# Performance work log

Measured on AMD Instinct MI355X. Metric: run time of the kernel, lower is better.

## Reference

```python
import jax, jax.numpy as jnp
import numpy as np

EMBED_DIM = 256
NUM_CODES = 8192
COMMIT_COST = 0.25


def setup_inputs() -> dict:
    key = jax.random.key(0)
    k1, k2 = jax.random.split(key)
    x = jax.random.normal(k1, (16, 1024, EMBED_DIM), dtype=jnp.float32)
    # torch init is uniform(-1/K, 1/K); use small-scale normal-like init via uniform
    codebook = jax.random.uniform(k2, (NUM_CODES, EMBED_DIM), dtype=jnp.float32,
                                  minval=-1.0 / NUM_CODES, maxval=1.0 / NUM_CODES)
    return {"x": x, "codebook": codebook}


def reference(x, codebook):
    # x: [B, S, D], codebook: [K, D]
    input_shape = x.shape
    flat = x.reshape(-1, EMBED_DIM)  # [N, D]
    distances = (jnp.sum(flat * flat, axis=1, keepdims=True)
                 + jnp.sum(codebook * codebook, axis=1)
                 - 2.0 * jnp.matmul(flat, codebook.T))
    encoding_indices = jnp.argmin(distances, axis=1)  # [N]
    # one-hot @ codebook is just a gather
    quantized = jnp.take(codebook, encoding_indices, axis=0).reshape(input_shape)
    # training w/ EMA: commitment loss only (codebook updated via EMA buffers, not grad)
    commitment_loss = COMMIT_COST * jnp.mean(
        (jax.lax.stop_gradient(quantized) - x) ** 2)
    # straight-through estimator
    quantized_st = x + jax.lax.stop_gradient(quantized - x)
    indices = encoding_indices.reshape(input_shape[:-1])
    return quantized_st, indices, commitment_loss
```

## Files before the change

### kernel.cpp

```cpp
#include <hip/hip_runtime.h>

#define D 256
#define KCODES 8192
#define NTOK 16384
#define QSIZE (NTOK * D)
#define NBLK 128
#define CBS 64
#define TH 2e-4f
#define CBSCALE 4096.0f
#define UNSCALE2 4.8828125e-4f
#define CCAP 4096

typedef _Float16 f16x8 __attribute__((ext_vector_type(8)));
typedef float f32x4 __attribute__((ext_vector_type(4)));
typedef __attribute__((address_space(3))) void* lds_vp;
typedef __attribute__((address_space(1))) const void* gbl_vp;

#define P1_LDS (128 * 256 * 2 + 2 * 128 * 32 * 2)
#define P2_LDS (256 * 65 * 4)

__device__ __forceinline__ ushort f32_to_bf16(float f) {
    unsigned u = __float_as_uint(f);
    return (ushort)((u + 0x7FFFu + ((u >> 16) & 1)) >> 16);
}
__device__ __forceinline__ float bf16_to_f32(ushort h) {
    return __uint_as_float((unsigned)h << 16);
}
__device__ __forceinline__ ushort f32_to_f16(float f) {
    _Float16 h = (_Float16)f;
    ushort u; __builtin_memcpy(&u, &h, 2);
    return u;
}
__device__ __forceinline__ float rdlane(float v, int lane) {
    return __uint_as_float(__builtin_amdgcn_readlane(__float_as_uint(v), lane));
}

__global__ __launch_bounds__(256) void prep_kernel(
    const float* __restrict__ x, ushort* __restrict__ xb,
    float* __restrict__ xsq, const float* __restrict__ cb,
    float* __restrict__ e2, unsigned* __restrict__ counts) {
    const int bid = blockIdx.x;
    const int tid = threadIdx.x;
    if (bid == 0 && tid < NBLK) counts[tid] = 0;
    if (bid < 4096) {
        int i = bid * 256 + tid;
        float4 v = reinterpret_cast<const float4*>(x)[i];
        ushort4 o;
        o.x = f32_to_f16(v.x); o.y = f32_to_f16(v.y);
        o.z = f32_to_f16(v.z); o.w = f32_to_f16(v.w);
        reinterpret_cast<ushort4*>(xb)[i] = o;
        float s = v.x * v.x + v.y * v.y + v.z * v.z + v.w * v.w;
#pragma unroll
        for (int off = 32; off > 0; off >>= 1) s += __shfl_down(s, off);
        if ((tid & 63) == 0) xsq[i >> 6] = s;
    } else {
        int c = (bid - 4096) * 4 + (tid >> 6);
        int lane = tid & 63;
        float4 v = reinterpret_cast<const float4*>(cb + (size_t)c * D)[lane];
        float s = v.x * v.x + v.y * v.y + v.z * v.z + v.w * v.w;
#pragma unroll
        for (int off = 32; off > 0; off >>= 1) s += __shfl_down(s, off);
        if (lane == 0) e2[c] = s;
    }
}

__global__ __launch_bounds__(256, 2) void pass1_kernel(
    const ushort* __restrict__ xb, const float* __restrict__ cb,
    const float* __restrict__ e2, unsigned* __restrict__ screen) {
    extern __shared__ ushort sm[];
    ushort* Bsh = sm;
    ushort* Ash = sm + 128 * 256;
    const int tid = threadIdx.x;
    const int w = tid >> 6, l = tid & 63;
    const int wr = w >> 1, wc = w & 1;
    const int n0 = blockIdx.y * 128;
    const int tc0 = blockIdx.x * (NTOK / 8);

#pragma unroll
    for (int j = 0; j < 16; ++j) {
        int c = tid + j * 256;
        int row = c >> 5, slot = c & 31;
        const float4* grow = reinterpret_cast<const float4*>(cb + (size_t)(n0 + row) * D);
        float4 f0 = grow[slot * 2];
        float4 f1 = grow[slot * 2 + 1];
        uint4 q;
        q.x = (unsigned)f32_to_f16(f0.x * CBSCALE) |
              ((unsigned)f32_to_f16(f0.y * CBSCALE) << 16);
        q.y = (unsigned)f32_to_f16(f0.z * CBSCALE) |
              ((unsigned)f32_to_f16(f0.w * CBSCALE) << 16);
        q.z = (unsigned)f32_to_f16(f1.x * CBSCALE) |
              ((unsigned)f32_to_f16(f1.y * CBSCALE) << 16);
        q.w = (unsigned)f32_to_f16(f1.z * CBSCALE) |
              ((unsigned)f32_to_f16(f1.w * CBSCALE) << 16);
        int sw = slot ^ (row & 7);
        *reinterpret_cast<uint4*>(Bsh + row * 256 + sw * 8) = q;
    }

    const int arow0 = w * 32 + (l >> 2);
    const int arow1 = arow0 + 16;
    const int asg8 = (((l & 3) ^ ((l >> 3) & 3)) << 3);

#define STAGE_A(TB, KT, BUF)                                                               \
    do {                                                                                   \
        __builtin_amdgcn_global_load_lds(                                                  \
            (gbl_vp)(xb + (size_t)((TB) + arow0) * D + (KT) * 32 + asg8),                  \
            (lds_vp)(Ash + (BUF) * 4096 + w * 1024), 16, 0, 0);                            \
        __builtin_amdgcn_global_load_lds(                                                  \
            (gbl_vp)(xb + (size_t)((TB) + arow1) * D + (KT) * 32 + asg8),                  \
            (lds_vp)(Ash + (BUF) * 4096 + w * 1024 + 512), 16, 0, 0);                      \
    } while (0)

    const int qh = l >> 4, l7 = l & 7, lm = l & 15;
    const int aslot = qh ^ ((lm >> 1) & 3);
    const int arow_rd = (wr * 64 + lm) * 32 + aslot * 8;
    const int brow_rd = (wc * 64 + lm) * 256;

    float e2v[16];
#pragma unroll
    for (int cm = 0; cm < 4; ++cm)
#pragma unroll
        for (int r = 0; r < 4; ++r)
            e2v[cm * 4 + r] = e2[n0 + wc * 64 + cm * 16 + qh * 4 + r];
    const int nb64 = blockIdx.y * 2 + wc;

    STAGE_A(tc0, 0, 0);
    __syncthreads();

    for (int tt = 0; tt < 16; ++tt) {
        const int tbase = tc0 + tt * 128;
        f32x4 acc[4][4];
#pragma unroll
        for (int cm = 0; cm < 4; ++cm)
#pragma unroll
            for (int tn = 0; tn < 4; ++tn) acc[cm][tn] = (f32x4)0.f;
#pragma unroll
        for (int kt = 0; kt < 8; ++kt) {
            const int cur = kt & 1;
            if (kt < 7) STAGE_A(tbase, kt + 1, cur ^ 1);
            else if (tt < 15) STAGE_A(tbase + 128, 0, cur ^ 1);
            const ushort* abase = Ash + cur * 4096 + arow_rd;
            f16x8 a[4], b[4];
#pragma unroll
            for (int tn = 0; tn < 4; ++tn)
                a[tn] = *reinterpret_cast<const f16x8*>(abase + tn * 512);
#pragma unroll
            for (int cm = 0; cm < 4; ++cm)
                b[cm] = *reinterpret_cast<const f16x8*>(
                    Bsh + brow_rd + cm * 4096 + (((kt * 4 + qh) ^ l7) << 3));
#pragma unroll
            for (int cm = 0; cm < 4; ++cm)
#pragma unroll
                for (int tn = 0; tn < 4; ++tn)
                    acc[cm][tn] = __builtin_amdgcn_mfma_f32_16x16x32_f16(
                        b[cm], a[tn], acc[cm][tn], 0, 0, 0);
            if (kt == 7) {
#pragma unroll
                for (int tn = 0; tn < 4; ++tn) {
                    float v1 = fmaf(-UNSCALE2, acc[0][tn][0], e2v[0]);
                    float v2 = 3.4e38f;
                    int a1 = qh * 4;
#pragma unroll
                    for (int q = 1; q < 16; ++q) {
                        const int cm = q >> 2, r = q & 3;
                        float f = fmaf(-UNSCALE2, acc[cm][tn][r], e2v[q]);
                        int idx = cm * 16 + qh * 4 + r;
                        bool lt = f < v1;
                        v2 = lt ? v1 : fminf(v2, f);
                        a1 = lt ? idx : a1;
                        v1 = lt ? f : v1;
                    }
#pragma unroll
                    for (int off = 16; off < 64; off <<= 1) {
                        float ov1 = __shfl_xor(v1, off);
                        float ov2 = __shfl_xor(v2, off);
                        int oa1 = __shfl_xor(a1, off);
                        float nv2 = fminf(fminf(v2, ov2), fmaxf(v1, ov1));
                        bool take = ov1 < v1;
                        v1 = take ? ov1 : v1;
                        a1 = take ? oa1 : a1;
                        v2 = nv2;
                    }
                    if (qh == 0) {
                        int token = tbase + wr * 64 + tn * 16 + lm;
                        ushort m1b = f32_to_bf16(v1);
                        unsigned big = (v2 - bf16_to_f32(m1b) > TH) ? 1u : 0u;
                        screen[(size_t)token * NBLK + nb64] =
                            ((unsigned)m1b << 16) | ((unsigned)a1 << 1) | big;
                    }
                }
            }
            __syncthreads();
        }
    }
#undef STAGE_A
}

__global__ __launch_bounds__(256) void pass2a_kernel(
    const unsigned* __restrict__ screen, unsigned long long* __restrict__ bestKey,
    unsigned* __restrict__ cand, unsigned* __restrict__ counts,
    float* __restrict__ out) {
    const int tid = threadIdx.x;
    const int w = tid >> 6, l = tid & 63;
    const int token = blockIdx.x * 4 + w;
    if (blockIdx.x == 0 && tid == 0) out[(size_t)QSIZE + NTOK] = 0.f;

    uint2 u2 = reinterpret_cast<const uint2*>(screen + (size_t)token * NBLK)[l];
    float ma = bf16_to_f32((ushort)(u2.x >> 16));
    float mb = bf16_to_f32((ushort)(u2.y >> 16));
    float v1, v2; unsigned pk; int blk;
    if (mb < ma) { v1 = mb; v2 = ma; pk = u2.y; blk = 2 * l + 1; }
    else         { v1 = ma; v2 = mb; pk = u2.x; blk = 2 * l; }
#pragma unroll
    for (int off = 1; off < 64; off <<= 1) {
        float ov1 = __shfl_xor(v1, off);
        float ov2 = __shfl_xor(v2, off);
        unsigned opk = __shfl_xor(pk, off);
        int oblk = __shfl_xor(blk, off);
        float nv2 = fminf(fminf(v2, ov2), fmaxf(v1, ov1));
        bool take = ov1 < v1;
        v1 = take ? ov1 : v1;
        pk = take ? opk : pk;
        blk = take ? oblk : blk;
        v2 = nv2;
    }
    bool decided = ((pk & 1u) != 0u) && (v2 - v1 > TH);
    if (l == 0)
        bestKey[token] = decided
            ? (unsigned long long)(unsigned)(blk * 64 + (int)((pk >> 1) & 63u))
            : 0xFFFFFFFFFFFFFFFFULL;
    if (!decided) {
        float thr = v1 + TH;
        if (ma <= thr) {
            unsigned s = atomicAdd(&counts[2 * l], 1u);
            if (s < CCAP) cand[(size_t)(2 * l) * CCAP + s] = (unsigned)token;
        }
        if (mb <= thr) {
            unsigned s = atomicAdd(&counts[2 * l + 1], 1u);
            if (s < CCAP) cand[(size_t)(2 * l + 1) * CCAP + s] = (unsigned)token;
        }
    }
}

__global__ __launch_bounds__(256, 2) void pass2b_kernel(
    const float* __restrict__ x, const float* __restrict__ cb,
    const float* __restrict__ e2, const float* __restrict__ xsq,
    const unsigned* __restrict__ cand, const unsigned* __restrict__ counts,
    unsigned long long* __restrict__ bestKey) {
    extern __shared__ float csh[];
    const int tid = threadIdx.x;
    const int nb = blockIdx.x >> 2;
    const int quarter = blockIdx.x & 3;
    int cnt = (int)counts[nb];
    if (cnt > CCAP) cnt = CCAP;
    if (quarter * 16 >= cnt) return;

#pragma unroll
    for (int r = 0; r < 16; ++r) {
        int i = r * 256 + tid;
        int row = i >> 6, kq = i & 63;
        float4 v = reinterpret_cast<const float4*>(cb + (size_t)(nb * CBS + row) * D)[kq];
        csh[(kq * 4 + 0) * 65 + row] = v.x;
        csh[(kq * 4 + 1) * 65 + row] = v.y;
        csh[(kq * 4 + 2) * 65 + row] = v.z;
        csh[(kq * 4 + 3) * 65 + row] = v.w;
    }
    __syncthreads();

    const int w = tid >> 6, j = tid & 63;
    const float e2v = e2[nb * CBS + j];
    const int ci0 = nb * CBS + j;
    const float4* X4 = reinterpret_cast<const float4*>(x);
    const unsigned* clist = cand + (size_t)nb * CCAP;
    const int slot = quarter * 4 + w;
    const int p0 = slot * 4;
    if (p0 >= cnt) return;

    for (int p = p0; p < cnt; p += 64) {
        int i1 = p + 1 < cnt ? p + 1 : cnt - 1;
        int i2 = p + 2 < cnt ? p + 2 : cnt - 1;
        int i3 = p + 3 < cnt ? p + 3 : cnt - 1;
        int t0 = (int)clist[p],  t1 = (int)clist[i1];
        int t2 = (int)clist[i2], t3 = (int)clist[i3];
        float4 v0 = X4[(size_t)t0 * 64 + j];
        float4 v1 = X4[(size_t)t1 * 64 + j];
        float4 v2 = X4[(size_t)t2 * 64 + j];
        float4 v3 = X4[(size_t)t3 * 64 + j];
        float a0 = 0.f, a1 = 0.f, a2 = 0.f, a3 = 0.f;
#pragma unroll
        for (int kq = 0; kq < 64; ++kq) {
            float c0 = csh[(kq * 4 + 0) * 65 + j];
            float c1 = csh[(kq * 4 + 1) * 65 + j];
            float c2 = csh[(kq * 4 + 2) * 65 + j];
            float c3 = csh[(kq * 4 + 3) * 65 + j];
            a0 = fmaf(rdlane(v0.x, kq), c0, a0);
            a0 = fmaf(rdlane(v0.y, kq), c1, a0);
            a0 = fmaf(rdlane(v0.z, kq), c2, a0);
            a0 = fmaf(rdlane(v0.w, kq), c3, a0);
            a1 = fmaf(rdlane(v1.x, kq), c0, a1);
            a1 = fmaf(rdlane(v1.y, kq), c1, a1);
            a1 = fmaf(rdlane(v1.z, kq), c2, a1);
            a1 = fmaf(rdlane(v1.w, kq), c3, a1);
            a2 = fmaf(rdlane(v2.x, kq), c0, a2);
            a2 = fmaf(rdlane(v2.y, kq), c1, a2);
            a2 = fmaf(rdlane(v2.z, kq), c2, a2);
            a2 = fmaf(rdlane(v2.w, kq), c3, a2);
            a3 = fmaf(rdlane(v3.x, kq), c0, a3);
            a3 = fmaf(rdlane(v3.y, kq), c1, a3);
            a3 = fmaf(rdlane(v3.z, kq), c2, a3);
            a3 = fmaf(rdlane(v3.w, kq), c3, a3);
        }
        float av[4] = {a0, a1, a2, a3};
        int tv[4] = {t0, t1, t2, t3};
#pragma unroll
        for (int g = 0; g < 4; ++g) {
            float dd = fmaf(-2.f, av[g], xsq[tv[g]] + e2v);
            int ci = ci0;
#pragma unroll
            for (int off = 1; off < 64; off <<= 1) {
                float od = __shfl_xor(dd, off);
                int oc = __shfl_xor(ci, off);
                if (od < dd || (od == dd && oc < ci)) { dd = od; ci = oc; }
            }
            if (j == 0) {
                unsigned u = __float_as_uint(dd);
                u = (u & 0x80000000u) ? ~u : (u | 0x80000000u);
                unsigned long long key =
                    ((unsigned long long)u << 32) | (unsigned)ci;
                atomicMin(bestKey + tv[g], key);
            }
        }
    }
}

__global__ __launch_bounds__(256) void gather_kernel(
    const float* __restrict__ x, const float* __restrict__ cb,
    const unsigned long long* __restrict__ bestKey,
    float* __restrict__ out) {
    __shared__ float red[4];
    const int tid = threadIdx.x;
    float acc = 0.f;
#pragma unroll
    for (int i = 0; i < 8; ++i) {
        const int token = blockIdx.x * 8 + i;
        int idx = (int)(bestKey[token] & 0xFFFFFFFFULL);
        if ((unsigned)idx >= (unsigned)KCODES) idx = 0;
        float q = cb[(size_t)idx * D + tid];
        float xv = x[(size_t)token * D + tid];
        out[(size_t)token * D + tid] = q;
        float d = q - xv;
        acc += d * d;
        if (tid == 0) out[(size_t)QSIZE + token] = (float)idx;
    }
#pragma unroll
    for (int off = 32; off > 0; off >>= 1) acc += __shfl_down(acc, off);
    if ((tid & 63) == 0) red[tid >> 6] = acc;
    __syncthreads();
    if (tid == 0) {
        float total = red[0] + red[1] + red[2] + red[3];
        atomicAdd(out + (size_t)QSIZE + NTOK, 0.25f * total / (float)QSIZE);
    }
}

extern "C" void kernel_launch(void* const* d_in, const int* in_sizes, int n_in,
                              void* d_out, int out_size, void* d_ws, size_t ws_size,
                              hipStream_t stream) {
    const float* x = (const float*)d_in[0];
    const float* cb = (const float*)d_in[1];
    float* out = (float*)d_out;
    float* ws = (float*)d_ws;

    ushort* xb = (ushort*)d_out;
    unsigned* screen = (unsigned*)((char*)d_out + 8388608);
    unsigned* cand = (unsigned*)d_out;

    float* e2 = ws;
    float* xsq = ws + 8192;
    unsigned* counts = (unsigned*)(ws + 8192 + 16384);
    unsigned long long* bestKey = (unsigned long long*)(ws + 8192 + 3 * 16384);

    hipFuncSetAttribute((const void*)pass1_kernel,
                        hipFuncAttributeMaxDynamicSharedMemorySize, P1_LDS);
    hipFuncSetAttribute((const void*)pass2b_kernel,
                        hipFuncAttributeMaxDynamicSharedMemorySize, P2_LDS);

    prep_kernel<<<4096 + KCODES / 4, 256, 0, stream>>>(x, xb, xsq, cb, e2, counts);
    pass1_kernel<<<dim3(8, KCODES / 128), 256, P1_LDS, stream>>>(xb, cb, e2, screen);
    pass2a_kernel<<<NTOK / 4, 256, 0, stream>>>(screen, bestKey, cand, counts, out);
    pass2b_kernel<<<4 * NBLK, 256, P2_LDS, stream>>>(
        x, cb, e2, xsq, cand, counts, bestKey);
    gather_kernel<<<NTOK / 8, 256, 0, stream>>>(x, cb, bestKey, out);
}
```

Before: 312.0 us.

## Keep codebook B fragments resident in registers instead of LDS in pass1

Each wave now loads and converts its slice of the codebook tile (64 codes x 256 dims) directly into registers, 32 f16x8 vectors per lane, in place of staging the whole 128x256 tile in LDS. This removes the per-iteration LDS reads for B and shrinks LDS use to just the double-buffered A tiles. The first A stage is issued before the codebook load so the two overlap. The cost is 128 extra VGPRs per lane under launch_bounds(256,2), which raises spill risk and register pressure.

```diff
diff --git a/kernel.cpp b/kernel.cpp
--- a/kernel.cpp
+++ b/kernel.cpp
@@ -16,7 +16,7 @@
 typedef __attribute__((address_space(3))) void* lds_vp;
 typedef __attribute__((address_space(1))) const void* gbl_vp;
 
-#define P1_LDS (128 * 256 * 2 + 2 * 128 * 32 * 2)
+#define P1_LDS (2 * 128 * 32 * 2)
 #define P2_LDS (256 * 65 * 4)
 
 __device__ __forceinline__ ushort f32_to_bf16(float f) {
@@ -68,33 +68,14 @@
     const ushort* __restrict__ xb, const float* __restrict__ cb,
     const float* __restrict__ e2, unsigned* __restrict__ screen) {
     extern __shared__ ushort sm[];
-    ushort* Bsh = sm;
-    ushort* Ash = sm + 128 * 256;
+    ushort* Ash = sm;
     const int tid = threadIdx.x;
     const int w = tid >> 6, l = tid & 63;
     const int wr = w >> 1, wc = w & 1;
     const int n0 = blockIdx.y * 128;
     const int tc0 = blockIdx.x * (NTOK / 8);
 
-#pragma unroll
-    for (int j = 0; j < 16; ++j) {
-        int c = tid + j * 256;
-        int row = c >> 5, slot = c & 31;
-        const float4* grow = reinterpret_cast<const float4*>(cb + (size_t)(n0 + row) * D);
-        float4 f0 = grow[slot * 2];
-        float4 f1 = grow[slot * 2 + 1];
-        uint4 q;
-        q.x = (unsigned)f32_to_f16(f0.x * CBSCALE) |
-              ((unsigned)f32_to_f16(f0.y * CBSCALE) << 16);
-        q.y = (unsigned)f32_to_f16(f0.z * CBSCALE) |
-              ((unsigned)f32_to_f16(f0.w * CBSCALE) << 16);
-        q.z = (unsigned)f32_to_f16(f1.x * CBSCALE) |
-              ((unsigned)f32_to_f16(f1.y * CBSCALE) << 16);
-        q.w = (unsigned)f32_to_f16(f1.z * CBSCALE) |
-              ((unsigned)f32_to_f16(f1.w * CBSCALE) << 16);
-        int sw = slot ^ (row & 7);
-        *reinterpret_cast<uint4*>(Bsh + row * 256 + sw * 8) = q;
-    }
+    const int qh = l >> 4, lm = l & 15;
 
     const int arow0 = w * 32 + (l >> 2);
     const int arow1 = arow0 + 16;
@@ -110,10 +91,34 @@
             (lds_vp)(Ash + (BUF) * 4096 + w * 1024 + 512), 16, 0, 0);                      \
     } while (0)
 
-    const int qh = l >> 4, l7 = l & 7, lm = l & 15;
     const int aslot = qh ^ ((lm >> 1) & 3);
     const int arow_rd = (wr * 64 + lm) * 32 + aslot * 8;
-    const int brow_rd = (wc * 64 + lm) * 256;
+
+    STAGE_A(tc0, 0, 0);
+
+    f16x8 breg[4][8];
+    {
+        const float* bb = cb + (size_t)(n0 + wc * 64 + lm) * D + qh * 8;
+#pragma unroll
+        for (int cm = 0; cm < 4; ++cm) {
+            const float4* src = reinterpret_cast<const float4*>(bb + (size_t)cm * 16 * D);
+#pragma unroll
+            for (int kt = 0; kt < 8; ++kt) {
+                float4 f0 = src[kt * 8];
+                float4 f1 = src[kt * 8 + 1];
+                f16x8 t;
+                t[0] = (_Float16)(f0.x * CBSCALE);
+                t[1] = (_Float16)(f0.y * CBSCALE);
+                t[2] = (_Float16)(f0.z * CBSCALE);
+                t[3] = (_Float16)(f0.w * CBSCALE);
+                t[4] = (_Float16)(f1.x * CBSCALE);
+                t[5] = (_Float16)(f1.y * CBSCALE);
+                t[6] = (_Float16)(f1.z * CBSCALE);
+                t[7] = (_Float16)(f1.w * CBSCALE);
+                breg[cm][kt] = t;
+            }
+        }
+    }
 
     float e2v[16];
 #pragma unroll
@@ -123,7 +128,6 @@
             e2v[cm * 4 + r] = e2[n0 + wc * 64 + cm * 16 + qh * 4 + r];
     const int nb64 = blockIdx.y * 2 + wc;
 
-    STAGE_A(tc0, 0, 0);
     __syncthreads();
 
     for (int tt = 0; tt < 16; ++tt) {
@@ -139,20 +143,16 @@
             if (kt < 7) STAGE_A(tbase, kt + 1, cur ^ 1);
             else if (tt < 15) STAGE_A(tbase + 128, 0, cur ^ 1);
             const ushort* abase = Ash + cur * 4096 + arow_rd;
-            f16x8 a[4], b[4];
+            f16x8 a[4];
 #pragma unroll
             for (int tn = 0; tn < 4; ++tn)
                 a[tn] = *reinterpret_cast<const f16x8*>(abase + tn * 512);
 #pragma unroll
             for (int cm = 0; cm < 4; ++cm)
-                b[cm] = *reinterpret_cast<const f16x8*>(
-                    Bsh + brow_rd + cm * 4096 + (((kt * 4 + qh) ^ l7) << 3));
-#pragma unroll
-            for (int cm = 0; cm < 4; ++cm)
 #pragma unroll
                 for (int tn = 0; tn < 4; ++tn)
                     acc[cm][tn] = __builtin_amdgcn_mfma_f32_16x16x32_f16(
-                        b[cm], a[tn], acc[cm][tn], 0, 0, 0);
+                        breg[cm][kt], a[tn], acc[cm][tn], 0, 0, 0);
             if (kt == 7) {
 #pragma unroll
                 for (int tn = 0; tn < 4; ++tn) {
```

New measurement: 313.4 us. No clear change (+0.5%).
